# Kernel tuning notes

Measured on AMD Instinct MI355X. Metric: run time of the kernel, lower is better.

## Reference

```python
import jax, jax.numpy as jnp
import numpy as np

MAX_DEG = 6


def neighbor_lookup(atoms, edges, maskvalue, include_self):
    # atoms: (B, A, F), edges: (B, A, D) with -1 padding
    B, A, F = atoms.shape
    D = edges.shape[-1]
    mask = edges >= 0
    idx = jnp.where(mask, edges, 0).reshape(B, A * D)
    g = jnp.take_along_axis(atoms, idx[:, :, None], axis=1).reshape(B, A, D, F)
    g = jnp.where(mask[..., None], g, maskvalue)
    if include_self:
        g = jnp.concatenate([atoms[:, :, None, :], g], axis=2)  # (B,A,D+1,F)
    return g


def graph_conv(atoms, bonds, edges, W, b):
    # W: (MAX_DEG, F_in+BF, C), b: (MAX_DEG, C)
    deg = (edges >= 0).sum(-1)  # (B, A)
    summed_atoms = neighbor_lookup(atoms, edges, 0.0, True).sum(2)  # self + neighbors
    summed_bonds = bonds.sum(2)
    feats = jnp.concatenate([summed_atoms, summed_bonds], axis=-1)
    out = jnp.zeros(feats.shape[:2] + (W.shape[-1],), feats.dtype)
    for d in range(MAX_DEG):  # small fixed loop over degrees
        h = jax.nn.relu(feats @ W[d] + b[d])
        out = out + jnp.where((deg == d)[..., None], h, 0.0)
    return out


def graph_pool(atoms, edges):
    g = neighbor_lookup(atoms, edges, -jnp.inf, True)  # self included -> finite max
    return g.max(axis=2)


def graph_output(atoms, bonds, edges, Wo, bo):
    deg = (edges >= 0).sum(-1)
    feats = jnp.concatenate([atoms, bonds.sum(2)], axis=-1)
    out = jax.nn.softmax(feats @ Wo + bo, axis=-1)
    mask = (deg != 0)[..., None]  # zero out padded atoms
    return jnp.where(mask, out, 0.0).sum(axis=1)  # (B, hid)


def setup_inputs():
    key = jax.random.key(0)
    ks = jax.random.split(key, 16)
    B, A, D = 4096, 64, 6
    AF, BF, H = 37, 6, 128
    s = lambda k, sh: (jax.random.normal(k, sh, jnp.float32) * 0.05)
    return {
        "atoms": jax.random.normal(ks[0], (B, A, AF), jnp.float32),
        "bonds": jax.random.normal(ks[1], (B, A, D, BF), jnp.float32),
        "edges": jax.random.randint(ks[2], (B, A, D), -1, A),
        "W1": s(ks[3], (MAX_DEG, AF + BF, H)),
        "b1": s(ks[4], (MAX_DEG, H)),
        "W2": s(ks[5], (MAX_DEG, H + BF, H)),
        "b2": s(ks[6], (MAX_DEG, H)),
        "Wo": s(ks[7], (H + BF, H)),
        "bo": s(ks[8], (H,)),
        "Wm1": s(ks[9], (H, H // 2)),
        "bm1": s(ks[10], (H // 2,)),
        "Wm2": s(ks[11], (H // 2, H // 4)),
        "bm2": s(ks[12], (H // 4,)),
        "Wm3": s(ks[13], (H // 4, 1)),
        "bm3": s(ks[14], (1,)),
    }


def reference(atoms, bonds, edges, W1, b1, W2, b2, Wo, bo, Wm1, bm1, Wm2, bm2, Wm3, bm3):
    x = graph_conv(atoms, bonds, edges, W1, b1)
    x = graph_pool(x, edges)
    x = graph_conv(x, bonds, edges, W2, b2)
    x = graph_pool(x, edges)
    fp = graph_output(x, bonds, edges, Wo, bo)
    h = jax.nn.relu(fp @ Wm1 + bm1)
    h = jax.nn.relu(h @ Wm2 + bm2)
    out = (h @ Wm3 + bm3).squeeze()  # (B,)
    return out
```

## Files before the change

### kernel.cpp

```cpp
#include <hip/hip_runtime.h>
#include <math.h>


__device__ __forceinline__ float4 max4(float4 a, float4 b) {
  return make_float4(fmaxf(a.x, b.x), fmaxf(a.y, b.y), fmaxf(a.z, b.z), fmaxf(a.w, b.w));
}

__device__ __forceinline__ float4 nbr_max(const float4* sx4, const int* se, int a, int c4) {
  float4 m = sx4[a * 32 + c4];
#pragma unroll
  for (int d = 0; d < 6; ++d) {
    int e = se[a * 6 + d];
    if (e >= 0) m = max4(m, sx4[e * 32 + c4]);
  }
  return m;
}

__device__ __forceinline__ float4 nbr_sum(const float4* sx4, const int* se, int a, int c4) {
  float4 s = sx4[a * 32 + c4];
#pragma unroll
  for (int d = 0; d < 6; ++d) {
    int e = se[a * 6 + d];
    if (e >= 0) {
      float4 v = sx4[e * 32 + c4];
      s.x += v.x; s.y += v.y; s.z += v.z; s.w += v.w;
    }
  }
  return s;
}

__device__ __forceinline__ float4 nbr_wmax(const float4* sx4, const int* se, const int* sdeg,
                                           int a, int c4) {
  float4 m = make_float4(0.f, 0.f, 0.f, 0.f);
  if (sdeg[a] < 6) m = max4(m, sx4[a * 32 + c4]);
#pragma unroll
  for (int d = 0; d < 6; ++d) {
    int e = se[a * 6 + d];
    if (e >= 0 && sdeg[e] < 6) m = max4(m, sx4[e * 32 + c4]);
  }
  return m;
}

__global__ __launch_bounds__(256, 4) void qsar_fused(
    const float* __restrict__ atoms, const float* __restrict__ bonds,
    const int* __restrict__ edges,
    const float* __restrict__ W1, const float* __restrict__ b1,
    const float* __restrict__ W2, const float* __restrict__ b2,
    const float* __restrict__ Wo, const float* __restrict__ bo,
    const float* __restrict__ Wm1, const float* __restrict__ bm1,
    const float* __restrict__ Wm2, const float* __restrict__ bm2,
    const float* __restrict__ Wm3, const float* __restrict__ bm3,
    float* __restrict__ out)
{
  const int b    = blockIdx.x;
  const int tid  = threadIdx.x;
  const int wid  = tid >> 6;
  const int hid  = tid >> 5;
  const int hl   = tid & 31;

  __shared__ float s_x[64 * 128];
  __shared__ float s_sa[16 * 38];
  __shared__ float s_bsum[64 * 8];
  __shared__ int   s_edges[64 * 6];
  __shared__ int   s_deg[64];
  __shared__ int   s_work[64];
  __shared__ int   s_perm[64];
  __shared__ float s_rsum[64];
  __shared__ int   s_nwork, s_na, s_nz;

  float4* sx4  = reinterpret_cast<float4*>(s_x);
  float*  s_fp = s_sa;
  float*  s_h1 = s_sa + 256;
  float*  s_h2 = s_sa + 320;

  {
    const int* ge = edges + (size_t)b * (64 * 6);
    for (int i = tid; i < 64 * 6; i += 256) s_edges[i] = ge[i];
    const float* gb = bonds + (size_t)b * (64 * 36);
    for (int i = tid; i < 64 * 6; i += 256) {
      int a = i / 6, f = i - a * 6;
      float s = 0.f;
#pragma unroll
      for (int d = 0; d < 6; ++d) s += gb[a * 36 + d * 6 + f];
      s_bsum[a * 8 + f] = s;
    }
#pragma unroll
    for (int j = 0; j < 8; ++j) sx4[tid + j * 256] = make_float4(0.f, 0.f, 0.f, 0.f);
    if (tid == 0) { s_nwork = 0; s_na = 0; s_nz = 0; }
  }
  __syncthreads();

  if (tid < 64) {
    int dcnt = 0;
#pragma unroll
    for (int d = 0; d < 6; ++d) dcnt += (s_edges[tid * 6 + d] >= 0) ? 1 : 0;
    s_deg[tid] = dcnt;
    if (dcnt < 6) { int p = atomicAdd(&s_nwork, 1); s_work[p] = tid; }
  }
  __syncthreads();

  if (tid < 64) {
    int nzf = (s_deg[tid] < 6) ? 1 : 0;
#pragma unroll
    for (int d = 0; d < 6; ++d) {
      int e = s_edges[tid * 6 + d];
      if (e >= 0 && s_deg[e] < 6) nzf = 1;
    }
    if (nzf) { int p = atomicAdd(&s_na, 1); s_perm[p] = tid; }
    else     { int p = atomicAdd(&s_nz, 1); s_perm[63 - p] = tid; }
  }

  {
    const int nw = s_nwork;
    const float* ga = atoms + (size_t)b * (64 * 37);
    const int c0 = hl * 4;
    for (int cb = 0; cb < nw; cb += 16) {
      const int cnt = (nw - cb < 16) ? (nw - cb) : 16;
      for (int i = tid; i < cnt * 37; i += 256) {
        int wi = i / 37, k = i - wi * 37;
        int a = s_work[cb + wi];
        float f = ga[a * 37 + k];
#pragma unroll
        for (int d = 0; d < 6; ++d) {
          int e = s_edges[a * 6 + d];
          if (e >= 0) f += ga[e * 37 + k];
        }
        s_sa[wi * 38 + k] = f;
      }
      __syncthreads();
      for (int w = hid; w < cnt; w += 8) {
        const int a = s_work[cb + w];
        const int d = s_deg[a];
        const float* wp = W1 + d * (43 * 128);
        float4 acc = *reinterpret_cast<const float4*>(&b1[d * 128 + c0]);
#pragma unroll 4
        for (int k = 0; k < 37; ++k) {
          const float f = s_sa[w * 38 + k];
          const float4 w4 = *reinterpret_cast<const float4*>(&wp[k * 128 + c0]);
          acc.x = fmaf(f, w4.x, acc.x); acc.y = fmaf(f, w4.y, acc.y);
          acc.z = fmaf(f, w4.z, acc.z); acc.w = fmaf(f, w4.w, acc.w);
        }
#pragma unroll
        for (int kk = 0; kk < 6; ++kk) {
          const float f = s_bsum[a * 8 + kk];
          const float4 w4 = *reinterpret_cast<const float4*>(&wp[(37 + kk) * 128 + c0]);
          acc.x = fmaf(f, w4.x, acc.x); acc.y = fmaf(f, w4.y, acc.y);
          acc.z = fmaf(f, w4.z, acc.z); acc.w = fmaf(f, w4.w, acc.w);
        }
        *reinterpret_cast<float4*>(&s_x[a * 128 + c0]) =
            make_float4(fmaxf(acc.x, 0.f), fmaxf(acc.y, 0.f),
                        fmaxf(acc.z, 0.f), fmaxf(acc.w, 0.f));
      }
      __syncthreads();
    }
  }
  __syncthreads();

  {
    float4 v0 = nbr_max(sx4, s_edges, (tid + 0 * 256) >> 5, tid & 31);
    float4 v1 = nbr_max(sx4, s_edges, (tid + 1 * 256) >> 5, tid & 31);
    float4 v2 = nbr_max(sx4, s_edges, (tid + 2 * 256) >> 5, tid & 31);
    float4 v3 = nbr_max(sx4, s_edges, (tid + 3 * 256) >> 5, tid & 31);
    float4 v4 = nbr_max(sx4, s_edges, (tid + 4 * 256) >> 5, tid & 31);
    float4 v5 = nbr_max(sx4, s_edges, (tid + 5 * 256) >> 5, tid & 31);
    float4 v6 = nbr_max(sx4, s_edges, (tid + 6 * 256) >> 5, tid & 31);
    float4 v7 = nbr_max(sx4, s_edges, (tid + 7 * 256) >> 5, tid & 31);
    __syncthreads();
    sx4[tid + 0 * 256] = v0; sx4[tid + 1 * 256] = v1;
    sx4[tid + 2 * 256] = v2; sx4[tid + 3 * 256] = v3;
    sx4[tid + 4 * 256] = v4; sx4[tid + 5 * 256] = v5;
    sx4[tid + 6 * 256] = v6; sx4[tid + 7 * 256] = v7;
  }
  __syncthreads();

  {
    const float4 z = make_float4(0.f, 0.f, 0.f, 0.f);
    float4 v0 = z, v1 = z, v2 = z, v3 = z, v4 = z, v5 = z, v6 = z, v7 = z;
    if (s_deg[(tid + 0 * 256) >> 5] < 6) v0 = nbr_sum(sx4, s_edges, (tid + 0 * 256) >> 5, tid & 31);
    if (s_deg[(tid + 1 * 256) >> 5] < 6) v1 = nbr_sum(sx4, s_edges, (tid + 1 * 256) >> 5, tid & 31);
    if (s_deg[(tid + 2 * 256) >> 5] < 6) v2 = nbr_sum(sx4, s_edges, (tid + 2 * 256) >> 5, tid & 31);
    if (s_deg[(tid + 3 * 256) >> 5] < 6) v3 = nbr_sum(sx4, s_edges, (tid + 3 * 256) >> 5, tid & 31);
    if (s_deg[(tid + 4 * 256) >> 5] < 6) v4 = nbr_sum(sx4, s_edges, (tid + 4 * 256) >> 5, tid & 31);
    if (s_deg[(tid + 5 * 256) >> 5] < 6) v5 = nbr_sum(sx4, s_edges, (tid + 5 * 256) >> 5, tid & 31);
    if (s_deg[(tid + 6 * 256) >> 5] < 6) v6 = nbr_sum(sx4, s_edges, (tid + 6 * 256) >> 5, tid & 31);
    if (s_deg[(tid + 7 * 256) >> 5] < 6) v7 = nbr_sum(sx4, s_edges, (tid + 7 * 256) >> 5, tid & 31);
    __syncthreads();
    if (s_deg[(tid + 0 * 256) >> 5] < 6) sx4[tid + 0 * 256] = v0;
    if (s_deg[(tid + 1 * 256) >> 5] < 6) sx4[tid + 1 * 256] = v1;
    if (s_deg[(tid + 2 * 256) >> 5] < 6) sx4[tid + 2 * 256] = v2;
    if (s_deg[(tid + 3 * 256) >> 5] < 6) sx4[tid + 3 * 256] = v3;
    if (s_deg[(tid + 4 * 256) >> 5] < 6) sx4[tid + 4 * 256] = v4;
    if (s_deg[(tid + 5 * 256) >> 5] < 6) sx4[tid + 5 * 256] = v5;
    if (s_deg[(tid + 6 * 256) >> 5] < 6) sx4[tid + 6 * 256] = v6;
    if (s_deg[(tid + 7 * 256) >> 5] < 6) sx4[tid + 7 * 256] = v7;
  }
  __syncthreads();

  {
    const int nw = s_nwork;
    const int c0 = hl * 4;
    for (int w = hid; w < nw; w += 8) {
      const int a = s_work[w];
      const int d = s_deg[a];
      const float* wp = W2 + d * (134 * 128);
      float4 acc = *reinterpret_cast<const float4*>(&b2[d * 128 + c0]);
#pragma unroll 4
      for (int k = 0; k < 128; ++k) {
        const float f = s_x[a * 128 + k];
        const float4 w4 = *reinterpret_cast<const float4*>(&wp[k * 128 + c0]);
        acc.x = fmaf(f, w4.x, acc.x); acc.y = fmaf(f, w4.y, acc.y);
        acc.z = fmaf(f, w4.z, acc.z); acc.w = fmaf(f, w4.w, acc.w);
      }
#pragma unroll
      for (int kk = 0; kk < 6; ++kk) {
        const float f = s_bsum[a * 8 + kk];
        const float4 w4 = *reinterpret_cast<const float4*>(&wp[(128 + kk) * 128 + c0]);
        acc.x = fmaf(f, w4.x, acc.x); acc.y = fmaf(f, w4.y, acc.y);
        acc.z = fmaf(f, w4.z, acc.z); acc.w = fmaf(f, w4.w, acc.w);
      }
      *reinterpret_cast<float4*>(&s_x[a * 128 + c0]) =
          make_float4(fmaxf(acc.x, 0.f), fmaxf(acc.y, 0.f),
                      fmaxf(acc.z, 0.f), fmaxf(acc.w, 0.f));
    }
  }
  __syncthreads();

  {
    float4 v0 = nbr_wmax(sx4, s_edges, s_deg, (tid + 0 * 256) >> 5, tid & 31);
    float4 v1 = nbr_wmax(sx4, s_edges, s_deg, (tid + 1 * 256) >> 5, tid & 31);
    float4 v2 = nbr_wmax(sx4, s_edges, s_deg, (tid + 2 * 256) >> 5, tid & 31);
    float4 v3 = nbr_wmax(sx4, s_edges, s_deg, (tid + 3 * 256) >> 5, tid & 31);
    float4 v4 = nbr_wmax(sx4, s_edges, s_deg, (tid + 4 * 256) >> 5, tid & 31);
    float4 v5 = nbr_wmax(sx4, s_edges, s_deg, (tid + 5 * 256) >> 5, tid & 31);
    float4 v6 = nbr_wmax(sx4, s_edges, s_deg, (tid + 6 * 256) >> 5, tid & 31);
    float4 v7 = nbr_wmax(sx4, s_edges, s_deg, (tid + 7 * 256) >> 5, tid & 31);
    __syncthreads();
    sx4[tid + 0 * 256] = v0; sx4[tid + 1 * 256] = v1;
    sx4[tid + 2 * 256] = v2; sx4[tid + 3 * 256] = v3;
    sx4[tid + 4 * 256] = v4; sx4[tid + 5 * 256] = v5;
    sx4[tid + 6 * 256] = v6; sx4[tid + 7 * 256] = v7;
  }
  __syncthreads();

  {
    const int cg = tid & 31, ag = hid;
    const int c0 = cg * 4;
    const int na = s_na;
    const int nr = (na + 31) >> 5;
    for (int j = 0; j < nr; ++j) {
      const int sl = j * 32 + ag * 4;
      const int at0 = s_perm[sl + 0], at1 = s_perm[sl + 1];
      const int at2 = s_perm[sl + 2], at3 = s_perm[sl + 3];
      float a00 = 0.f, a01 = 0.f, a02 = 0.f, a03 = 0.f;
      float a10 = 0.f, a11 = 0.f, a12 = 0.f, a13 = 0.f;
      float a20 = 0.f, a21 = 0.f, a22 = 0.f, a23 = 0.f;
      float a30 = 0.f, a31 = 0.f, a32 = 0.f, a33 = 0.f;
      if (j * 32 + wid * 8 < na) {
#pragma unroll 4
        for (int k = 0; k < 128; ++k) {
          const float4 w4 = *reinterpret_cast<const float4*>(Wo + k * 128 + c0);
          const float f0 = s_x[at0 * 128 + k], f1 = s_x[at1 * 128 + k];
          const float f2 = s_x[at2 * 128 + k], f3 = s_x[at3 * 128 + k];
          a00 = fmaf(f0, w4.x, a00); a01 = fmaf(f0, w4.y, a01);
          a02 = fmaf(f0, w4.z, a02); a03 = fmaf(f0, w4.w, a03);
          a10 = fmaf(f1, w4.x, a10); a11 = fmaf(f1, w4.y, a11);
          a12 = fmaf(f1, w4.z, a12); a13 = fmaf(f1, w4.w, a13);
          a20 = fmaf(f2, w4.x, a20); a21 = fmaf(f2, w4.y, a21);
          a22 = fmaf(f2, w4.z, a22); a23 = fmaf(f2, w4.w, a23);
          a30 = fmaf(f3, w4.x, a30); a31 = fmaf(f3, w4.y, a31);
          a32 = fmaf(f3, w4.z, a32); a33 = fmaf(f3, w4.w, a33);
        }
#pragma unroll
        for (int kk = 0; kk < 6; ++kk) {
          const float4 w4 = *reinterpret_cast<const float4*>(Wo + (128 + kk) * 128 + c0);
          const float f0 = s_bsum[at0 * 8 + kk], f1 = s_bsum[at1 * 8 + kk];
          const float f2 = s_bsum[at2 * 8 + kk], f3 = s_bsum[at3 * 8 + kk];
          a00 = fmaf(f0, w4.x, a00); a01 = fmaf(f0, w4.y, a01);
          a02 = fmaf(f0, w4.z, a02); a03 = fmaf(f0, w4.w, a03);
          a10 = fmaf(f1, w4.x, a10); a11 = fmaf(f1, w4.y, a11);
          a12 = fmaf(f1, w4.z, a12); a13 = fmaf(f1, w4.w, a13);
          a20 = fmaf(f2, w4.x, a20); a21 = fmaf(f2, w4.y, a21);
          a22 = fmaf(f2, w4.z, a22); a23 = fmaf(f2, w4.w, a23);
          a30 = fmaf(f3, w4.x, a30); a31 = fmaf(f3, w4.y, a31);
          a32 = fmaf(f3, w4.z, a32); a33 = fmaf(f3, w4.w, a33);
        }
      }
      __syncthreads();
      const float4 bo4 = *reinterpret_cast<const float4*>(bo + c0);
      if (sl + 0 < na)
        *reinterpret_cast<float4*>(&s_x[at0 * 128 + c0]) =
            make_float4(a00 + bo4.x, a01 + bo4.y, a02 + bo4.z, a03 + bo4.w);
      if (sl + 1 < na)
        *reinterpret_cast<float4*>(&s_x[at1 * 128 + c0]) =
            make_float4(a10 + bo4.x, a11 + bo4.y, a12 + bo4.z, a13 + bo4.w);
      if (sl + 2 < na)
        *reinterpret_cast<float4*>(&s_x[at2 * 128 + c0]) =
            make_float4(a20 + bo4.x, a21 + bo4.y, a22 + bo4.z, a23 + bo4.w);
      if (sl + 3 < na)
        *reinterpret_cast<float4*>(&s_x[at3 * 128 + c0]) =
            make_float4(a30 + bo4.x, a31 + bo4.y, a32 + bo4.z, a33 + bo4.w);
    }
    const int nz = 64 - na;
    for (int e = tid; e < nz * 128; e += 256) {
      int zi = e >> 7, c = e & 127;
      int a = s_perm[na + zi];
      float acc = bo[c];
#pragma unroll
      for (int kk = 0; kk < 6; ++kk)
        acc = fmaf(s_bsum[a * 8 + kk], Wo[(128 + kk) * 128 + c], acc);
      s_x[a * 128 + c] = acc;
    }
  }
  __syncthreads();

  {
    const int a = tid >> 2, q = tid & 3;
    float* base = &s_x[a * 128 + q * 32];
    const float4 v0 = *reinterpret_cast<const float4*>(base + ((0 + tid) & 7) * 4);
    const float4 v1 = *reinterpret_cast<const float4*>(base + ((1 + tid) & 7) * 4);
    const float4 v2 = *reinterpret_cast<const float4*>(base + ((2 + tid) & 7) * 4);
    const float4 v3 = *reinterpret_cast<const float4*>(base + ((3 + tid) & 7) * 4);
    const float4 v4 = *reinterpret_cast<const float4*>(base + ((4 + tid) & 7) * 4);
    const float4 v5 = *reinterpret_cast<const float4*>(base + ((5 + tid) & 7) * 4);
    const float4 v6 = *reinterpret_cast<const float4*>(base + ((6 + tid) & 7) * 4);
    const float4 v7 = *reinterpret_cast<const float4*>(base + ((7 + tid) & 7) * 4);
    float mx = fmaxf(fmaxf(fmaxf(v0.x, v0.y), fmaxf(v0.z, v0.w)),
                     fmaxf(fmaxf(v1.x, v1.y), fmaxf(v1.z, v1.w)));
    mx = fmaxf(mx, fmaxf(fmaxf(fmaxf(v2.x, v2.y), fmaxf(v2.z, v2.w)),
                         fmaxf(fmaxf(v3.x, v3.y), fmaxf(v3.z, v3.w))));
    mx = fmaxf(mx, fmaxf(fmaxf(fmaxf(v4.x, v4.y), fmaxf(v4.z, v4.w)),
                         fmaxf(fmaxf(v5.x, v5.y), fmaxf(v5.z, v5.w))));
    mx = fmaxf(mx, fmaxf(fmaxf(fmaxf(v6.x, v6.y), fmaxf(v6.z, v6.w)),
                         fmaxf(fmaxf(v7.x, v7.y), fmaxf(v7.z, v7.w))));
    mx = fmaxf(mx, __shfl_xor(mx, 1));
    mx = fmaxf(mx, __shfl_xor(mx, 2));
    float sm = 0.f;
    float4 e0, e1, e2, e3, e4, e5, e6, e7;
    e0.x = __expf(v0.x - mx); e0.y = __expf(v0.y - mx); e0.z = __expf(v0.z - mx); e0.w = __expf(v0.w - mx);
    e1.x = __expf(v1.x - mx); e1.y = __expf(v1.y - mx); e1.z = __expf(v1.z - mx); e1.w = __expf(v1.w - mx);
    e2.x = __expf(v2.x - mx); e2.y = __expf(v2.y - mx); e2.z = __expf(v2.z - mx); e2.w = __expf(v2.w - mx);
    e3.x = __expf(v3.x - mx); e3.y = __expf(v3.y - mx); e3.z = __expf(v3.z - mx); e3.w = __expf(v3.w - mx);
    e4.x = __expf(v4.x - mx); e4.y = __expf(v4.y - mx); e4.z = __expf(v4.z - mx); e4.w = __expf(v4.w - mx);
    e5.x = __expf(v5.x - mx); e5.y = __expf(v5.y - mx); e5.z = __expf(v5.z - mx); e5.w = __expf(v5.w - mx);
    e6.x = __expf(v6.x - mx); e6.y = __expf(v6.y - mx); e6.z = __expf(v6.z - mx); e6.w = __expf(v6.w - mx);
    e7.x = __expf(v7.x - mx); e7.y = __expf(v7.y - mx); e7.z = __expf(v7.z - mx); e7.w = __expf(v7.w - mx);
    sm += e0.x + e0.y + e0.z + e0.w; sm += e1.x + e1.y + e1.z + e1.w;
    sm += e2.x + e2.y + e2.z + e2.w; sm += e3.x + e3.y + e3.z + e3.w;
    sm += e4.x + e4.y + e4.z + e4.w; sm += e5.x + e5.y + e5.z + e5.w;
    sm += e6.x + e6.y + e6.z + e6.w; sm += e7.x + e7.y + e7.z + e7.w;
    *reinterpret_cast<float4*>(base + ((0 + tid) & 7) * 4) = e0;
    *reinterpret_cast<float4*>(base + ((1 + tid) & 7) * 4) = e1;
    *reinterpret_cast<float4*>(base + ((2 + tid) & 7) * 4) = e2;
    *reinterpret_cast<float4*>(base + ((3 + tid) & 7) * 4) = e3;
    *reinterpret_cast<float4*>(base + ((4 + tid) & 7) * 4) = e4;
    *reinterpret_cast<float4*>(base + ((5 + tid) & 7) * 4) = e5;
    *reinterpret_cast<float4*>(base + ((6 + tid) & 7) * 4) = e6;
    *reinterpret_cast<float4*>(base + ((7 + tid) & 7) * 4) = e7;
    sm += __shfl_xor(sm, 1);
    sm += __shfl_xor(sm, 2);
    if (q == 0) s_rsum[a] = (s_deg[a] != 0) ? (1.f / sm) : 0.f;
  }
  __syncthreads();

  {
    const int c = tid & 127, half = tid >> 7;
    float s = 0.f;
    for (int a2 = half * 32; a2 < half * 32 + 32; ++a2)
      s = fmaf(s_x[a2 * 128 + c], s_rsum[a2], s);
    s_fp[half * 128 + c] = s;
  }
  __syncthreads();
  if (tid < 128) s_fp[tid] += s_fp[128 + tid];
  __syncthreads();

  if (tid < 64) {
    float acc = bm1[tid];
    for (int k = 0; k < 128; ++k) acc = fmaf(s_fp[k], Wm1[k * 64 + tid], acc);
    s_h1[tid] = fmaxf(acc, 0.f);
  }
  __syncthreads();
  if (tid < 32) {
    float acc = bm2[tid];
    for (int k = 0; k < 64; ++k) acc = fmaf(s_h1[k], Wm2[k * 32 + tid], acc);
    s_h2[tid] = fmaxf(acc, 0.f);
  }
  __syncthreads();
  if (tid < 64) {
    float p = (tid < 32) ? s_h2[tid] * Wm3[tid] : 0.f;
#pragma unroll
    for (int off = 32; off > 0; off >>= 1) p += __shfl_xor(p, off);
    if (tid == 0) out[b] = p + bm3[0];
  }
}

extern "C" void kernel_launch(void* const* d_in, const int* in_sizes, int n_in,
                              void* d_out, int out_size, void* d_ws, size_t ws_size,
                              hipStream_t stream) {
  const float* atoms = (const float*)d_in[0];
  const float* bonds = (const float*)d_in[1];
  const int*   edges = (const int*)d_in[2];
  const float* W1  = (const float*)d_in[3];
  const float* b1  = (const float*)d_in[4];
  const float* W2  = (const float*)d_in[5];
  const float* b2  = (const float*)d_in[6];
  const float* Wo  = (const float*)d_in[7];
  const float* bo  = (const float*)d_in[8];
  const float* Wm1 = (const float*)d_in[9];
  const float* bm1 = (const float*)d_in[10];
  const float* Wm2 = (const float*)d_in[11];
  const float* bm2 = (const float*)d_in[12];
  const float* Wm3 = (const float*)d_in[13];
  const float* bm3 = (const float*)d_in[14];
  float* out = (float*)d_out;

  const int B = out_size;
  qsar_fused<<<dim3(B), dim3(256), 0, stream>>>(
      atoms, bonds, edges, W1, b1, W2, b2, Wo, bo,
      Wm1, bm1, Wm2, bm2, Wm3, bm3, out);
}
```

Baseline: 245.8 us.

## Double block size to 512 threads and redistribute per-molecule work

Raises the fused per-molecule kernel from 256 to 512 threads. Every phase is re-split across twice as many threads: the gathers, both degree-specific matmuls, the pools, softmax (8 threads per atom) and the fingerprint reduction (four partial sums). The Wo stage now runs one pass over all 64 atoms with no masking on the k-loop result. The separate bias-only path for atoms with no contributing neighbours is gone; those atoms now get the bond term through the same path. This aims for more latency hiding per molecule, but launch_bounds(512,8) caps registers per thread, which may cause spills or lower achieved occupancy.

```diff
diff --git a/kernel.cpp b/kernel.cpp
--- a/kernel.cpp
+++ b/kernel.cpp
@@ -41,7 +41,7 @@
   return m;
 }
 
-__global__ __launch_bounds__(256, 4) void qsar_fused(
+__global__ __launch_bounds__(512, 8) void qsar_fused(
     const float* __restrict__ atoms, const float* __restrict__ bonds,
     const int* __restrict__ edges,
     const float* __restrict__ W1, const float* __restrict__ b1,
@@ -54,12 +54,11 @@
 {
   const int b    = blockIdx.x;
   const int tid  = threadIdx.x;
-  const int wid  = tid >> 6;
   const int hid  = tid >> 5;
   const int hl   = tid & 31;
 
   __shared__ float s_x[64 * 128];
-  __shared__ float s_sa[16 * 38];
+  __shared__ float s_sa[608];
   __shared__ float s_bsum[64 * 8];
   __shared__ int   s_edges[64 * 6];
   __shared__ int   s_deg[64];
@@ -70,14 +69,14 @@
 
   float4* sx4  = reinterpret_cast<float4*>(s_x);
   float*  s_fp = s_sa;
-  float*  s_h1 = s_sa + 256;
-  float*  s_h2 = s_sa + 320;
+  float*  s_h1 = s_sa + 512;
+  float*  s_h2 = s_sa + 576;
 
   {
     const int* ge = edges + (size_t)b * (64 * 6);
-    for (int i = tid; i < 64 * 6; i += 256) s_edges[i] = ge[i];
+    for (int i = tid; i < 64 * 6; i += 512) s_edges[i] = ge[i];
     const float* gb = bonds + (size_t)b * (64 * 36);
-    for (int i = tid; i < 64 * 6; i += 256) {
+    for (int i = tid; i < 64 * 6; i += 512) {
       int a = i / 6, f = i - a * 6;
       float s = 0.f;
 #pragma unroll
@@ -85,7 +84,7 @@
       s_bsum[a * 8 + f] = s;
     }
 #pragma unroll
-    for (int j = 0; j < 8; ++j) sx4[tid + j * 256] = make_float4(0.f, 0.f, 0.f, 0.f);
+    for (int j = 0; j < 4; ++j) sx4[tid + j * 512] = make_float4(0.f, 0.f, 0.f, 0.f);
     if (tid == 0) { s_nwork = 0; s_na = 0; s_nz = 0; }
   }
   __syncthreads();
@@ -116,7 +115,7 @@
     const int c0 = hl * 4;
     for (int cb = 0; cb < nw; cb += 16) {
       const int cnt = (nw - cb < 16) ? (nw - cb) : 16;
-      for (int i = tid; i < cnt * 37; i += 256) {
+      for (int i = tid; i < cnt * 37; i += 512) {
         int wi = i / 37, k = i - wi * 37;
         int a = s_work[cb + wi];
         float f = ga[a * 37 + k];
@@ -128,24 +127,24 @@
         s_sa[wi * 38 + k] = f;
       }
       __syncthreads();
-      for (int w = hid; w < cnt; w += 8) {
+      for (int w = hid; w < cnt; w += 16) {
         const int a = s_work[cb + w];
         const int d = s_deg[a];
-        const float* wp = W1 + d * (43 * 128);
+        const float4* wdf4 = reinterpret_cast<const float4*>(W1 + d * (43 * 128));
         float4 acc = *reinterpret_cast<const float4*>(&b1[d * 128 + c0]);
 #pragma unroll 4
         for (int k = 0; k < 37; ++k) {
-          const float f = s_sa[w * 38 + k];
-          const float4 w4 = *reinterpret_cast<const float4*>(&wp[k * 128 + c0]);
-          acc.x = fmaf(f, w4.x, acc.x); acc.y = fmaf(f, w4.y, acc.y);
-          acc.z = fmaf(f, w4.z, acc.z); acc.w = fmaf(f, w4.w, acc.w);
+          const float ff = s_sa[w * 38 + k];
+          const float4 w4 = wdf4[k * 32 + hl];
+          acc.x = fmaf(ff, w4.x, acc.x); acc.y = fmaf(ff, w4.y, acc.y);
+          acc.z = fmaf(ff, w4.z, acc.z); acc.w = fmaf(ff, w4.w, acc.w);
         }
 #pragma unroll
         for (int kk = 0; kk < 6; ++kk) {
-          const float f = s_bsum[a * 8 + kk];
-          const float4 w4 = *reinterpret_cast<const float4*>(&wp[(37 + kk) * 128 + c0]);
-          acc.x = fmaf(f, w4.x, acc.x); acc.y = fmaf(f, w4.y, acc.y);
-          acc.z = fmaf(f, w4.z, acc.z); acc.w = fmaf(f, w4.w, acc.w);
+          const float ff = s_bsum[a * 8 + kk];
+          const float4 w4 = wdf4[(37 + kk) * 32 + hl];
+          acc.x = fmaf(ff, w4.x, acc.x); acc.y = fmaf(ff, w4.y, acc.y);
+          acc.z = fmaf(ff, w4.z, acc.z); acc.w = fmaf(ff, w4.w, acc.w);
         }
         *reinterpret_cast<float4*>(&s_x[a * 128 + c0]) =
             make_float4(fmaxf(acc.x, 0.f), fmaxf(acc.y, 0.f),
@@ -157,66 +156,52 @@
   __syncthreads();
 
   {
-    float4 v0 = nbr_max(sx4, s_edges, (tid + 0 * 256) >> 5, tid & 31);
-    float4 v1 = nbr_max(sx4, s_edges, (tid + 1 * 256) >> 5, tid & 31);
-    float4 v2 = nbr_max(sx4, s_edges, (tid + 2 * 256) >> 5, tid & 31);
-    float4 v3 = nbr_max(sx4, s_edges, (tid + 3 * 256) >> 5, tid & 31);
-    float4 v4 = nbr_max(sx4, s_edges, (tid + 4 * 256) >> 5, tid & 31);
-    float4 v5 = nbr_max(sx4, s_edges, (tid + 5 * 256) >> 5, tid & 31);
-    float4 v6 = nbr_max(sx4, s_edges, (tid + 6 * 256) >> 5, tid & 31);
-    float4 v7 = nbr_max(sx4, s_edges, (tid + 7 * 256) >> 5, tid & 31);
+    float4 v0 = nbr_max(sx4, s_edges, (tid + 0 * 512) >> 5, tid & 31);
+    float4 v1 = nbr_max(sx4, s_edges, (tid + 1 * 512) >> 5, tid & 31);
+    float4 v2 = nbr_max(sx4, s_edges, (tid + 2 * 512) >> 5, tid & 31);
+    float4 v3 = nbr_max(sx4, s_edges, (tid + 3 * 512) >> 5, tid & 31);
     __syncthreads();
-    sx4[tid + 0 * 256] = v0; sx4[tid + 1 * 256] = v1;
-    sx4[tid + 2 * 256] = v2; sx4[tid + 3 * 256] = v3;
-    sx4[tid + 4 * 256] = v4; sx4[tid + 5 * 256] = v5;
-    sx4[tid + 6 * 256] = v6; sx4[tid + 7 * 256] = v7;
+    sx4[tid + 0 * 512] = v0; sx4[tid + 1 * 512] = v1;
+    sx4[tid + 2 * 512] = v2; sx4[tid + 3 * 512] = v3;
   }
   __syncthreads();
 
   {
     const float4 z = make_float4(0.f, 0.f, 0.f, 0.f);
-    float4 v0 = z, v1 = z, v2 = z, v3 = z, v4 = z, v5 = z, v6 = z, v7 = z;
-    if (s_deg[(tid + 0 * 256) >> 5] < 6) v0 = nbr_sum(sx4, s_edges, (tid + 0 * 256) >> 5, tid & 31);
-    if (s_deg[(tid + 1 * 256) >> 5] < 6) v1 = nbr_sum(sx4, s_edges, (tid + 1 * 256) >> 5, tid & 31);
-    if (s_deg[(tid + 2 * 256) >> 5] < 6) v2 = nbr_sum(sx4, s_edges, (tid + 2 * 256) >> 5, tid & 31);
-    if (s_deg[(tid + 3 * 256) >> 5] < 6) v3 = nbr_sum(sx4, s_edges, (tid + 3 * 256) >> 5, tid & 31);
-    if (s_deg[(tid + 4 * 256) >> 5] < 6) v4 = nbr_sum(sx4, s_edges, (tid + 4 * 256) >> 5, tid & 31);
-    if (s_deg[(tid + 5 * 256) >> 5] < 6) v5 = nbr_sum(sx4, s_edges, (tid + 5 * 256) >> 5, tid & 31);
-    if (s_deg[(tid + 6 * 256) >> 5] < 6) v6 = nbr_sum(sx4, s_edges, (tid + 6 * 256) >> 5, tid & 31);
-    if (s_deg[(tid + 7 * 256) >> 5] < 6) v7 = nbr_sum(sx4, s_edges, (tid + 7 * 256) >> 5, tid & 31);
+    float4 v0 = z, v1 = z, v2 = z, v3 = z;
+    if (s_deg[(tid + 0 * 512) >> 5] < 6) v0 = nbr_sum(sx4, s_edges, (tid + 0 * 512) >> 5, tid & 31);
+    if (s_deg[(tid + 1 * 512) >> 5] < 6) v1 = nbr_sum(sx4, s_edges, (tid + 1 * 512) >> 5, tid & 31);
+    if (s_deg[(tid + 2 * 512) >> 5] < 6) v2 = nbr_sum(sx4, s_edges, (tid + 2 * 512) >> 5, tid & 31);
+    if (s_deg[(tid + 3 * 512) >> 5] < 6) v3 = nbr_sum(sx4, s_edges, (tid + 3 * 512) >> 5, tid & 31);
     __syncthreads();
-    if (s_deg[(tid + 0 * 256) >> 5] < 6) sx4[tid + 0 * 256] = v0;
-    if (s_deg[(tid + 1 * 256) >> 5] < 6) sx4[tid + 1 * 256] = v1;
-    if (s_deg[(tid + 2 * 256) >> 5] < 6) sx4[tid + 2 * 256] = v2;
-    if (s_deg[(tid + 3 * 256) >> 5] < 6) sx4[tid + 3 * 256] = v3;
-    if (s_deg[(tid + 4 * 256) >> 5] < 6) sx4[tid + 4 * 256] = v4;
-    if (s_deg[(tid + 5 * 256) >> 5] < 6) sx4[tid + 5 * 256] = v5;
-    if (s_deg[(tid + 6 * 256) >> 5] < 6) sx4[tid + 6 * 256] = v6;
-    if (s_deg[(tid + 7 * 256) >> 5] < 6) sx4[tid + 7 * 256] = v7;
+    if (s_deg[(tid + 0 * 512) >> 5] < 6) sx4[tid + 0 * 512] = v0;
+    if (s_deg[(tid + 1 * 512) >> 5] < 6) sx4[tid + 1 * 512] = v1;
+    if (s_deg[(tid + 2 * 512) >> 5] < 6) sx4[tid + 2 * 512] = v2;
+    if (s_deg[(tid + 3 * 512) >> 5] < 6) sx4[tid + 3 * 512] = v3;
   }
   __syncthreads();
 
   {
     const int nw = s_nwork;
     const int c0 = hl * 4;
-    for (int w = hid; w < nw; w += 8) {
+    for (int w = hid; w < nw; w += 16) {
       const int a = s_work[w];
       const int d = s_deg[a];
-      const float* wp = W2 + d * (134 * 128);
+      const float4* wdf4 = reinterpret_cast<const float4*>(W2 + d * (134 * 128));
       float4 acc = *reinterpret_cast<const float4*>(&b2[d * 128 + c0]);
 #pragma unroll 4
       for (int k = 0; k < 128; ++k) {
-        const float f = s_x[a * 128 + k];
-        const float4 w4 = *reinterpret_cast<const float4*>(&wp[k * 128 + c0]);
-        acc.x = fmaf(f, w4.x, acc.x); acc.y = fmaf(f, w4.y, acc.y);
-        acc.z = fmaf(f, w4.z, acc.z); acc.w = fmaf(f, w4.w, acc.w);
+        const float ff = s_x[a * 128 + k];
+        const float4 w4 = wdf4[k * 32 + hl];
+        acc.x = fmaf(ff, w4.x, acc.x); acc.y = fmaf(ff, w4.y, acc.y);
+        acc.z = fmaf(ff, w4.z, acc.z); acc.w = fmaf(ff, w4.w, acc.w);
       }
 #pragma unroll
       for (int kk = 0; kk < 6; ++kk) {
-        const float f = s_bsum[a * 8 + kk];
-        const float4 w4 = *reinterpret_cast<const float4*>(&wp[(128 + kk) * 128 + c0]);
-        acc.x = fmaf(f, w4.x, acc.x); acc.y = fmaf(f, w4.y, acc.y);
-        acc.z = fmaf(f, w4.z, acc.z); acc.w = fmaf(f, w4.w, acc.w);
+        const float ff = s_bsum[a * 8 + kk];
+        const float4 w4 = wdf4[(128 + kk) * 32 + hl];
+        acc.x = fmaf(ff, w4.x, acc.x); acc.y = fmaf(ff, w4.y, acc.y);
+        acc.z = fmaf(ff, w4.z, acc.z); acc.w = fmaf(ff, w4.w, acc.w);
       }
       *reinterpret_cast<float4*>(&s_x[a * 128 + c0]) =
           make_float4(fmaxf(acc.x, 0.f), fmaxf(acc.y, 0.f),
@@ -226,151 +211,112 @@
   __syncthreads();
 
   {
-    float4 v0 = nbr_wmax(sx4, s_edges, s_deg, (tid + 0 * 256) >> 5, tid & 31);
-    float4 v1 = nbr_wmax(sx4, s_edges, s_deg, (tid + 1 * 256) >> 5, tid & 31);
-    float4 v2 = nbr_wmax(sx4, s_edges, s_deg, (tid + 2 * 256) >> 5, tid & 31);
-    float4 v3 = nbr_wmax(sx4, s_edges, s_deg, (tid + 3 * 256) >> 5, tid & 31);
-    float4 v4 = nbr_wmax(sx4, s_edges, s_deg, (tid + 4 * 256) >> 5, tid & 31);
-    float4 v5 = nbr_wmax(sx4, s_edges, s_deg, (tid + 5 * 256) >> 5, tid & 31);
-    float4 v6 = nbr_wmax(sx4, s_edges, s_deg, (tid + 6 * 256) >> 5, tid & 31);
-    float4 v7 = nbr_wmax(sx4, s_edges, s_deg, (tid + 7 * 256) >> 5, tid & 31);
+    float4 v0 = nbr_wmax(sx4, s_edges, s_deg, (tid + 0 * 512) >> 5, tid & 31);
+    float4 v1 = nbr_wmax(sx4, s_edges, s_deg, (tid + 1 * 512) >> 5, tid & 31);
+    float4 v2 = nbr_wmax(sx4, s_edges, s_deg, (tid + 2 * 512) >> 5, tid & 31);
+    float4 v3 = nbr_wmax(sx4, s_edges, s_deg, (tid + 3 * 512) >> 5, tid & 31);
     __syncthreads();
-    sx4[tid + 0 * 256] = v0; sx4[tid + 1 * 256] = v1;
-    sx4[tid + 2 * 256] = v2; sx4[tid + 3 * 256] = v3;
-    sx4[tid + 4 * 256] = v4; sx4[tid + 5 * 256] = v5;
-    sx4[tid + 6 * 256] = v6; sx4[tid + 7 * 256] = v7;
-  }
-  __syncthreads();
-
-  {
-    const int cg = tid & 31, ag = hid;
-    const int c0 = cg * 4;
+    sx4[tid + 0 * 512] = v0; sx4[tid + 1 * 512] = v1;
+    sx4[tid + 2 * 512] = v2; sx4[tid + 3 * 512] = v3;
+  }
+  __syncthreads();
+
+  {
+    const int c0 = hl * 4;
     const int na = s_na;
-    const int nr = (na + 31) >> 5;
-    for (int j = 0; j < nr; ++j) {
-      const int sl = j * 32 + ag * 4;
-      const int at0 = s_perm[sl + 0], at1 = s_perm[sl + 1];
-      const int at2 = s_perm[sl + 2], at3 = s_perm[sl + 3];
-      float a00 = 0.f, a01 = 0.f, a02 = 0.f, a03 = 0.f;
-      float a10 = 0.f, a11 = 0.f, a12 = 0.f, a13 = 0.f;
-      float a20 = 0.f, a21 = 0.f, a22 = 0.f, a23 = 0.f;
-      float a30 = 0.f, a31 = 0.f, a32 = 0.f, a33 = 0.f;
-      if (j * 32 + wid * 8 < na) {
+    const int sl = hid * 4;
+    const int at0 = s_perm[sl + 0], at1 = s_perm[sl + 1];
+    const int at2 = s_perm[sl + 2], at3 = s_perm[sl + 3];
+    float a00 = 0.f, a01 = 0.f, a02 = 0.f, a03 = 0.f;
+    float a10 = 0.f, a11 = 0.f, a12 = 0.f, a13 = 0.f;
+    float a20 = 0.f, a21 = 0.f, a22 = 0.f, a23 = 0.f;
+    float a30 = 0.f, a31 = 0.f, a32 = 0.f, a33 = 0.f;
+    const float4* Wof4 = reinterpret_cast<const float4*>(Wo);
+    if (sl < na) {
 #pragma unroll 4
-        for (int k = 0; k < 128; ++k) {
-          const float4 w4 = *reinterpret_cast<const float4*>(Wo + k * 128 + c0);
-          const float f0 = s_x[at0 * 128 + k], f1 = s_x[at1 * 128 + k];
-          const float f2 = s_x[at2 * 128 + k], f3 = s_x[at3 * 128 + k];
-          a00 = fmaf(f0, w4.x, a00); a01 = fmaf(f0, w4.y, a01);
-          a02 = fmaf(f0, w4.z, a02); a03 = fmaf(f0, w4.w, a03);
-          a10 = fmaf(f1, w4.x, a10); a11 = fmaf(f1, w4.y, a11);
-          a12 = fmaf(f1, w4.z, a12); a13 = fmaf(f1, w4.w, a13);
-          a20 = fmaf(f2, w4.x, a20); a21 = fmaf(f2, w4.y, a21);
-          a22 = fmaf(f2, w4.z, a22); a23 = fmaf(f2, w4.w, a23);
-          a30 = fmaf(f3, w4.x, a30); a31 = fmaf(f3, w4.y, a31);
-          a32 = fmaf(f3, w4.z, a32); a33 = fmaf(f3, w4.w, a33);
-        }
-#pragma unroll
-        for (int kk = 0; kk < 6; ++kk) {
-          const float4 w4 = *reinterpret_cast<const float4*>(Wo + (128 + kk) * 128 + c0);
-          const float f0 = s_bsum[at0 * 8 + kk], f1 = s_bsum[at1 * 8 + kk];
-          const float f2 = s_bsum[at2 * 8 + kk], f3 = s_bsum[at3 * 8 + kk];
-          a00 = fmaf(f0, w4.x, a00); a01 = fmaf(f0, w4.y, a01);
-          a02 = fmaf(f0, w4.z, a02); a03 = fmaf(f0, w4.w, a03);
-          a10 = fmaf(f1, w4.x, a10); a11 = fmaf(f1, w4.y, a11);
-          a12 = fmaf(f1, w4.z, a12); a13 = fmaf(f1, w4.w, a13);
-          a20 = fmaf(f2, w4.x, a20); a21 = fmaf(f2, w4.y, a21);
-          a22 = fmaf(f2, w4.z, a22); a23 = fmaf(f2, w4.w, a23);
-          a30 = fmaf(f3, w4.x, a30); a31 = fmaf(f3, w4.y, a31);
-          a32 = fmaf(f3, w4.z, a32); a33 = fmaf(f3, w4.w, a33);
-        }
-      }
-      __syncthreads();
-      const float4 bo4 = *reinterpret_cast<const float4*>(bo + c0);
-      if (sl + 0 < na)
-        *reinterpret_cast<float4*>(&s_x[at0 * 128 + c0]) =
-            make_float4(a00 + bo4.x, a01 + bo4.y, a02 + bo4.z, a03 + bo4.w);
-      if (sl + 1 < na)
-        *reinterpret_cast<float4*>(&s_x[at1 * 128 + c0]) =
-            make_float4(a10 + bo4.x, a11 + bo4.y, a12 + bo4.z, a13 + bo4.w);
-      if (sl + 2 < na)
-        *reinterpret_cast<float4*>(&s_x[at2 * 128 + c0]) =
-            make_float4(a20 + bo4.x, a21 + bo4.y, a22 + bo4.z, a23 + bo4.w);
-      if (sl + 3 < na)
-        *reinterpret_cast<float4*>(&s_x[at3 * 128 + c0]) =
-            make_float4(a30 + bo4.x, a31 + bo4.y, a32 + bo4.z, a33 + bo4.w);
-    }
-    const int nz = 64 - na;
-    for (int e = tid; e < nz * 128; e += 256) {
-      int zi = e >> 7, c = e & 127;
-      int a = s_perm[na + zi];
-      float acc = bo[c];
-#pragma unroll
-      for (int kk = 0; kk < 6; ++kk)
-        acc = fmaf(s_bsum[a * 8 + kk], Wo[(128 + kk) * 128 + c], acc);
-      s_x[a * 128 + c] = acc;
-    }
-  }
-  __syncthreads();
-
-  {
-    const int a = tid >> 2, q = tid & 3;
-    float* base = &s_x[a * 128 + q * 32];
-    const float4 v0 = *reinterpret_cast<const float4*>(base + ((0 + tid) & 7) * 4);
-    const float4 v1 = *reinterpret_cast<const float4*>(base + ((1 + tid) & 7) * 4);
-    const float4 v2 = *reinterpret_cast<const float4*>(base + ((2 + tid) & 7) * 4);
-    const float4 v3 = *reinterpret_cast<const float4*>(base + ((3 + tid) & 7) * 4);
-    const float4 v4 = *reinterpret_cast<const float4*>(base + ((4 + tid) & 7) * 4);
-    const float4 v5 = *reinterpret_cast<const float4*>(base + ((5 + tid) & 7) * 4);
-    const float4 v6 = *reinterpret_cast<const float4*>(base + ((6 + tid) & 7) * 4);
-    const float4 v7 = *reinterpret_cast<const float4*>(base + ((7 + tid) & 7) * 4);
+      for (int k = 0; k < 128; ++k) {
+        const float4 w4 = Wof4[k * 32 + hl];
+        const float f0 = s_x[at0 * 128 + k], f1 = s_x[at1 * 128 + k];
+        const float f2 = s_x[at2 * 128 + k], f3 = s_x[at3 * 128 + k];
+        a00 = fmaf(f0, w4.x, a00); a01 = fmaf(f0, w4.y, a01);
+        a02 = fmaf(f0, w4.z, a02); a03 = fmaf(f0, w4.w, a03);
+        a10 = fmaf(f1, w4.x, a10); a11 = fmaf(f1, w4.y, a11);
+        a12 = fmaf(f1, w4.z, a12); a13 = fmaf(f1, w4.w, a13);
+        a20 = fmaf(f2, w4.x, a20); a21 = fmaf(f2, w4.y, a21);
+        a22 = fmaf(f2, w4.z, a22); a23 = fmaf(f2, w4.w, a23);
+        a30 = fmaf(f3, w4.x, a30); a31 = fmaf(f3, w4.y, a31);
+        a32 = fmaf(f3, w4.z, a32); a33 = fmaf(f3, w4.w, a33);
+      }
+    }
+#pragma unroll
+    for (int kk = 0; kk < 6; ++kk) {
+      const float4 w4 = Wof4[(128 + kk) * 32 + hl];
+      const float f0 = s_bsum[at0 * 8 + kk], f1 = s_bsum[at1 * 8 + kk];
+      const float f2 = s_bsum[at2 * 8 + kk], f3 = s_bsum[at3 * 8 + kk];
+      a00 = fmaf(f0, w4.x, a00); a01 = fmaf(f0, w4.y, a01);
+      a02 = fmaf(f0, w4.z, a02); a03 = fmaf(f0, w4.w, a03);
+      a10 = fmaf(f1, w4.x, a10); a11 = fmaf(f1, w4.y, a11);
+      a12 = fmaf(f1, w4.z, a12); a13 = fmaf(f1, w4.w, a13);
+      a20 = fmaf(f2, w4.x, a20); a21 = fmaf(f2, w4.y, a21);
+      a22 = fmaf(f2, w4.z, a22); a23 = fmaf(f2, w4.w, a23);
+      a30 = fmaf(f3, w4.x, a30); a31 = fmaf(f3, w4.y, a31);
+      a32 = fmaf(f3, w4.z, a32); a33 = fmaf(f3, w4.w, a33);
+    }
+    const float4 bo4 = *reinterpret_cast<const float4*>(bo + c0);
+    *reinterpret_cast<float4*>(&s_x[at0 * 128 + c0]) =
+        make_float4(a00 + bo4.x, a01 + bo4.y, a02 + bo4.z, a03 + bo4.w);
+    *reinterpret_cast<float4*>(&s_x[at1 * 128 + c0]) =
+        make_float4(a10 + bo4.x, a11 + bo4.y, a12 + bo4.z, a13 + bo4.w);
+    *reinterpret_cast<float4*>(&s_x[at2 * 128 + c0]) =
+        make_float4(a20 + bo4.x, a21 + bo4.y, a22 + bo4.z, a23 + bo4.w);
+    *reinterpret_cast<float4*>(&s_x[at3 * 128 + c0]) =
+        make_float4(a30 + bo4.x, a31 + bo4.y, a32 + bo4.z, a33 + bo4.w);
+  }
+  __syncthreads();
+
+  {
+    const int a = tid >> 3, q = tid & 7;
+    float* base = &s_x[a * 128 + q * 16];
+    const float4 v0 = *reinterpret_cast<const float4*>(base + ((0 + tid) & 3) * 4);
+    const float4 v1 = *reinterpret_cast<const float4*>(base + ((1 + tid) & 3) * 4);
+    const float4 v2 = *reinterpret_cast<const float4*>(base + ((2 + tid) & 3) * 4);
+    const float4 v3 = *reinterpret_cast<const float4*>(base + ((3 + tid) & 3) * 4);
     float mx = fmaxf(fmaxf(fmaxf(v0.x, v0.y), fmaxf(v0.z, v0.w)),
                      fmaxf(fmaxf(v1.x, v1.y), fmaxf(v1.z, v1.w)));
     mx = fmaxf(mx, fmaxf(fmaxf(fmaxf(v2.x, v2.y), fmaxf(v2.z, v2.w)),
                          fmaxf(fmaxf(v3.x, v3.y), fmaxf(v3.z, v3.w))));
-    mx = fmaxf(mx, fmaxf(fmaxf(fmaxf(v4.x, v4.y), fmaxf(v4.z, v4.w)),
-                         fmaxf(fmaxf(v5.x, v5.y), fmaxf(v5.z, v5.w))));
-    mx = fmaxf(mx, fmaxf(fmaxf(fmaxf(v6.x, v6.y), fmaxf(v6.z, v6.w)),
-                         fmaxf(fmaxf(v7.x, v7.y), fmaxf(v7.z, v7.w))));
     mx = fmaxf(mx, __shfl_xor(mx, 1));
     mx = fmaxf(mx, __shfl_xor(mx, 2));
-    float sm = 0.f;
-    float4 e0, e1, e2, e3, e4, e5, e6, e7;
+    mx = fmaxf(mx, __shfl_xor(mx, 4));
+    float4 e0, e1, e2, e3;
     e0.x = __expf(v0.x - mx); e0.y = __expf(v0.y - mx); e0.z = __expf(v0.z - mx); e0.w = __expf(v0.w - mx);
     e1.x = __expf(v1.x - mx); e1.y = __expf(v1.y - mx); e1.z = __expf(v1.z - mx); e1.w = __expf(v1.w - mx);
     e2.x = __expf(v2.x - mx); e2.y = __expf(v2.y - mx); e2.z = __expf(v2.z - mx); e2.w = __expf(v2.w - mx);
     e3.x = __expf(v3.x - mx); e3.y = __expf(v3.y - mx); e3.z = __expf(v3.z - mx); e3.w = __expf(v3.w - mx);
-    e4.x = __expf(v4.x - mx); e4.y = __expf(v4.y - mx); e4.z = __expf(v4.z - mx); e4.w = __expf(v4.w - mx);
-    e5.x = __expf(v5.x - mx); e5.y = __expf(v5.y - mx); e5.z = __expf(v5.z - mx); e5.w = __expf(v5.w - mx);
-    e6.x = __expf(v6.x - mx); e6.y = __expf(v6.y - mx); e6.z = __expf(v6.z - mx); e6.w = __expf(v6.w - mx);
-    e7.x = __expf(v7.x - mx); e7.y = __expf(v7.y - mx); e7.z = __expf(v7.z - mx); e7.w = __expf(v7.w - mx);
-    sm += e0.x + e0.y + e0.z + e0.w; sm += e1.x + e1.y + e1.z + e1.w;
-    sm += e2.x + e2.y + e2.z + e2.w; sm += e3.x + e3.y + e3.z + e3.w;
-    sm += e4.x + e4.y + e4.z + e4.w; sm += e5.x + e5.y + e5.z + e5.w;
-    sm += e6.x + e6.y + e6.z + e6.w; sm += e7.x + e7.y + e7.z + e7.w;
-    *reinterpret_cast<float4*>(base + ((0 + tid) & 7) * 4) = e0;
-    *reinterpret_cast<float4*>(base + ((1 + tid) & 7) * 4) = e1;
-    *reinterpret_cast<float4*>(base + ((2 + tid) & 7) * 4) = e2;
-    *reinterpret_cast<float4*>(base + ((3 + tid) & 7) * 4) = e3;
-    *reinterpret_cast<float4*>(base + ((4 + tid) & 7) * 4) = e4;
-    *reinterpret_cast<float4*>(base + ((5 + tid) & 7) * 4) = e5;
-    *reinterpret_cast<float4*>(base + ((6 + tid) & 7) * 4) = e6;
-    *reinterpret_cast<float4*>(base + ((7 + tid) & 7) * 4) = e7;
+    float sm = e0.x + e0.y + e0.z + e0.w;
+    sm += e1.x + e1.y + e1.z + e1.w;
+    sm += e2.x + e2.y + e2.z + e2.w;
+    sm += e3.x + e3.y + e3.z + e3.w;
+    *reinterpret_cast<float4*>(base + ((0 + tid) & 3) * 4) = e0;
+    *reinterpret_cast<float4*>(base + ((1 + tid) & 3) * 4) = e1;
+    *reinterpret_cast<float4*>(base + ((2 + tid) & 3) * 4) = e2;
+    *reinterpret_cast<float4*>(base + ((3 + tid) & 3) * 4) = e3;
     sm += __shfl_xor(sm, 1);
     sm += __shfl_xor(sm, 2);
+    sm += __shfl_xor(sm, 4);
     if (q == 0) s_rsum[a] = (s_deg[a] != 0) ? (1.f / sm) : 0.f;
   }
   __syncthreads();
 
   {
-    const int c = tid & 127, half = tid >> 7;
+    const int c = tid & 127, quarter = tid >> 7;
     float s = 0.f;
-    for (int a2 = half * 32; a2 < half * 32 + 32; ++a2)
+    for (int a2 = quarter * 16; a2 < quarter * 16 + 16; ++a2)
       s = fmaf(s_x[a2 * 128 + c], s_rsum[a2], s);
-    s_fp[half * 128 + c] = s;
-  }
-  __syncthreads();
-  if (tid < 128) s_fp[tid] += s_fp[128 + tid];
+    s_fp[quarter * 128 + c] = s;
+  }
+  __syncthreads();
+  if (tid < 128) s_fp[tid] += s_fp[128 + tid] + s_fp[256 + tid] + s_fp[384 + tid];
   __syncthreads();
 
   if (tid < 64) {
@@ -414,7 +360,7 @@
   float* out = (float*)d_out;
 
   const int B = out_size;
-  qsar_fused<<<dim3(B), dim3(256), 0, stream>>>(
+  qsar_fused<<<dim3(B), dim3(512), 0, stream>>>(
       atoms, bonds, edges, W1, b1, W2, b2, Wo, bo,
       Wm1, bm1, Wm2, bm2, Wm3, bm3, out);
 }
```

New measurement: 238.9 us. -2.8%, faster.
